# Kernel tuning notes

Measured on AMD Instinct MI355X. Metric: run time of the kernel, lower is better.

## Reference

```python
import jax, jax.numpy as jnp
import numpy as np
import math

H = 2048          # hidden_size
NH = 16           # num_attn_heads
HD = H // NH      # attn head dim = 128
NFW = 4           # num_lact_heads
FD = H // NFW     # fw head dim = 512
DH = FD           # inter_multi = 1.0
CHUNK = 512       # lact_chunk_size
WINDOW = 2048     # window_size
ROPE_BASE = 500000.0
BASE_LR_INV = math.log(math.expm1(0.001))  # inv_softplus(1e-3)


def rmsnorm(x, w, eps=1e-6):
    return x * jax.lax.rsqrt(jnp.mean(x * x, axis=-1, keepdims=True) + eps) * w


def l2norm(x, eps=1e-12):
    return x * jax.lax.rsqrt(jnp.sum(x * x, axis=-1, keepdims=True) + eps)


def rope(x):  # x: [b, h, s, d], half-split convention
    d = x.shape[-1]
    s = x.shape[2]
    inv = 1.0 / (ROPE_BASE ** (jnp.arange(d // 2, dtype=jnp.float32) / (d // 2)))
    f = jnp.arange(s, dtype=jnp.float32)[:, None] * inv[None, :]  # [s, d/2]
    cos, sin = jnp.cos(f), jnp.sin(f)
    x1, x2 = x[..., : d // 2], x[..., d // 2:]
    return jnp.concatenate([x1 * cos - x2 * sin, x2 * cos + x1 * sin], axis=-1)


def setup_inputs() -> dict:
    key = jax.random.key(0)
    ks = jax.random.split(key, 8)
    b, s = 2, 2048
    return {
        "hidden_states": jax.random.normal(ks[0], (b, s, H), jnp.float32),
        "qkv_w": jax.random.normal(ks[1], (3 * H, H), jnp.float32) / math.sqrt(H),
        "q_norm_w": jnp.ones((H,), jnp.float32),
        "k_norm_w": jnp.ones((H,), jnp.float32),
        "qk_scale": jnp.ones((H, 2), jnp.float32),
        "qk_offset": jnp.zeros((H, 2), jnp.float32),
        "lr_w": jax.random.normal(ks[2], (3 * NFW, H), jnp.float32) / math.sqrt(H),
        "lr_b": jnp.zeros((3 * NFW,), jnp.float32),
        "w0": jax.random.normal(ks[3], (NFW, DH, FD), jnp.float32) / math.sqrt(FD),
        "w1": jax.random.normal(ks[4], (NFW, FD, DH), jnp.float32) / math.sqrt(DH),
        "w2": jax.random.normal(ks[5], (NFW, DH, FD), jnp.float32) / math.sqrt(FD),
        "ttt_norm_w": jnp.ones((FD,), jnp.float32),
        "o_proj_w": jax.random.normal(ks[6], (H, H), jnp.float32) / math.sqrt(H),
    }


def reference(hidden_states, qkv_w, q_norm_w, k_norm_w, qk_scale, qk_offset,
              lr_w, lr_b, w0, w1, w2, ttt_norm_w, o_proj_w):
    x = hidden_states
    b, s, _ = x.shape
    nc = s // CHUNK

    qkv = x @ qkv_w.T
    q, k, v = jnp.split(qkv, 3, axis=-1)
    q = rmsnorm(q, q_norm_w)
    k = rmsnorm(k, k_norm_w)

    # ---- TTT (fast-weight SwiGLU) branch ----
    fq = jax.nn.silu(q * qk_scale[:, 0] + qk_offset[:, 0])
    fk = jax.nn.silu(k * qk_scale[:, 1] + qk_offset[:, 1])
    fv = jax.nn.silu(v)
    tohead = lambda t: t.reshape(b, s, NFW, FD).transpose(0, 2, 1, 3)  # [b,h,s,d]
    fq, fk, fv = l2norm(tohead(fq)), l2norm(tohead(fk)), tohead(fv)

    lr = jax.nn.softplus(x @ lr_w.T + lr_b + BASE_LR_INV)          # [b,s,3*NFW]
    lr = lr.reshape(b, s, 3, NFW).transpose(2, 0, 3, 1)[..., None]  # [3,b,h,s,1]
    lr0, lr1, lr2 = lr[0], lr[1], lr[2]

    chunkify = lambda t: t.reshape(b, NFW, nc, CHUNK, -1).transpose(2, 0, 1, 3, 4)
    qs, ks_, vs = chunkify(fq), chunkify(fk), chunkify(fv)
    l0s, l1s, l2s = chunkify(lr0), chunkify(lr1), chunkify(lr2)

    w0b = jnp.broadcast_to(w0, (b,) + w0.shape)
    w1b = jnp.broadcast_to(w1, (b,) + w1.shape)
    w2b = jnp.broadcast_to(w2, (b,) + w2.shape)

    def step(carry, xs):
        w0c, w1c, w2c = carry
        qc, kc, vc, l0, l1, l2 = xs
        # apply current fast weights to queries (strictly causal across chunks)
        hq = jax.nn.silu(jnp.einsum('bhcd,bhed->bhce', qc, w0c)) * \
             jnp.einsum('bhcd,bhed->bhce', qc, w2c)
        oc = jnp.einsum('bhce,bhde->bhcd', hq, w1c)
        # gradient-descent update on dot-product loss -sum(v * f(k))
        g1 = jnp.einsum('bhcd,bhed->bhce', kc, w0c)
        g2 = jnp.einsum('bhcd,bhed->bhce', kc, w2c)
        gate = jax.nn.silu(g1)
        hidden = gate * g2
        dhidden = jnp.einsum('bhcd,bhde->bhce', vc, w1c)  # w1^T v
        dh2 = dhidden * gate
        sig = jax.nn.sigmoid(g1)
        dh1 = dhidden * g2 * (sig * (1.0 + g1 * (1.0 - sig)))  # silu'(g1)
        w1n = w1c + jnp.einsum('bhcd,bhce->bhde', l1 * vc, hidden)
        w0n = w0c + jnp.einsum('bhce,bhcd->bhed', l0 * dh1, kc)
        w2n = w2c + jnp.einsum('bhce,bhcd->bhed', l2 * dh2, kc)
        return (w0n, w1n, w2n), oc

    _, o_chunks = jax.lax.scan(step, (w0b, w1b, w2b), (qs, ks_, vs, l0s, l1s, l2s))
    o_ttt = o_chunks.transpose(1, 2, 0, 3, 4).reshape(b, NFW, s, FD)
    o_ttt = rmsnorm(o_ttt, ttt_norm_w)
    o_ttt = o_ttt.transpose(0, 2, 1, 3).reshape(b, s, H)

    # ---- sliding-window attention branch ----
    qa = rope(q.reshape(b, s, NH, HD).transpose(0, 2, 1, 3))
    ka = rope(k.reshape(b, s, NH, HD).transpose(0, 2, 1, 3))
    va = v.reshape(b, s, NH, HD).transpose(0, 2, 1, 3)
    scores = jnp.einsum('bhqd,bhkd->bhqk', qa, ka) / math.sqrt(HD)
    i = jnp.arange(s)
    mask = (i[:, None] >= i[None, :]) & (i[:, None] - i[None, :] < WINDOW)
    scores = jnp.where(mask, scores, jnp.float32(-1e9))
    p = jax.nn.softmax(scores, axis=-1)
    attn = jnp.einsum('bhqk,bhkd->bhqd', p, va).transpose(0, 2, 1, 3).reshape(b, s, H)

    return (attn + o_ttt) @ o_proj_w.T
```

## Files before the change

### kernel.cpp

```cpp
#include <hip/hip_runtime.h>
#include <hip/hip_bf16.h>
#include <math.h>

using bf16 = __hip_bfloat16;

namespace {

constexpr int cH = 2048;
constexpr int cNH = 16;
constexpr int cHD = 128;
constexpr int cNFW = 4;
constexpr int cFD = 512;
constexpr int cS = 2048;
constexpr float cRSQRT_HD = 0.08838834764831845f;
constexpr long ZL_ = 262144;
constexpr long ZG_ = 1048576;

typedef __attribute__((ext_vector_type(8))) short short8;
typedef __attribute__((ext_vector_type(4))) float f32x4;

__device__ __forceinline__ float sigmoidf_(float x) { return 1.0f / (1.0f + __expf(-x)); }
__device__ __forceinline__ float b2f(bf16 v) { return __bfloat162float(v); }
__device__ __forceinline__ bf16 f2b(float v) { return __float2bfloat16(v); }
__device__ __forceinline__ unsigned short f2bu(float f) {
  return __builtin_bit_cast(unsigned short, __float2bfloat16(f));
}
__device__ __forceinline__ float bu2f(unsigned u) { return __uint_as_float(u << 16); }

#if defined(__has_builtin)
#if __has_builtin(__builtin_amdgcn_global_load_lds)
#define HAVE_GLOAD 1
#endif
#endif

__device__ __forceinline__ void gload16(const bf16* g, short* ldsbase) {
#ifdef HAVE_GLOAD
  __builtin_amdgcn_global_load_lds((const __attribute__((address_space(1))) void*)g,
                                   (__attribute__((address_space(3))) void*)ldsbase, 16, 0, 0);
#else
  const int l = threadIdx.x & 63;
  *(uint4*)(ldsbase + l * 8) = *(const uint4*)g;
#endif
}

__device__ __forceinline__ void stage16(const bf16* src, short* dst) {
  *(uint4*)dst = *(const uint4*)src;
  *(uint4*)(dst + 8) = *(const uint4*)(src + 8);
}

__device__ __forceinline__ void store1(float* p, float v) { *p = v; }
__device__ __forceinline__ void store1(bf16* p, float v) { *p = f2b(v); }

__device__ __forceinline__ void mm_core32(const bf16* __restrict__ Ab, int lda,
                                          const bf16* __restrict__ Bb, int ldb, int K,
                                          short* As, short* Bs, f32x4 acc[4][4]) {
  const int t = threadIdx.x, lane = t & 63, g = lane >> 4, c16 = lane & 15;
  const int wv = t >> 6, wm = (wv >> 1) * 64, wn = (wv & 1) * 64;
  for (int k0 = 0; k0 < K; k0 += 32) {
    __syncthreads();
    {
      const int ch = wv * 2;
      const bf16* ga = Ab + (size_t)(ch * 16 + (lane >> 2)) * lda + k0 + (lane & 3) * 8;
      gload16(ga, &As[ch * 512]);
      gload16(ga + (size_t)16 * lda, &As[ch * 512 + 512]);
      const bf16* gb = Bb + (size_t)(ch * 16 + (lane >> 2)) * ldb + k0 + (lane & 3) * 8;
      gload16(gb, &Bs[ch * 512]);
      gload16(gb + (size_t)16 * ldb, &Bs[ch * 512 + 512]);
    }
    __syncthreads();
    short8 af[4], bfr[4];
#pragma unroll
    for (int mi = 0; mi < 4; ++mi) af[mi] = *(const short8*)&As[(wm + mi * 16 + c16) * 32 + g * 8];
#pragma unroll
    for (int ni = 0; ni < 4; ++ni) bfr[ni] = *(const short8*)&Bs[(wn + ni * 16 + c16) * 32 + g * 8];
#pragma unroll
    for (int mi = 0; mi < 4; ++mi)
#pragma unroll
      for (int ni = 0; ni < 4; ++ni)
        acc[mi][ni] = __builtin_amdgcn_mfma_f32_16x16x32_bf16(af[mi], bfr[ni], acc[mi][ni], 0, 0, 0);
  }
}

template <bool ACC, bool MIR, typename TC>
__device__ __forceinline__ void mm_store(TC* Cb, bf16* Mb, int ldc, int rb, int cb, f32x4 acc[4][4]) {
  const int t = threadIdx.x, lane = t & 63, g = lane >> 4, c16 = lane & 15;
  const int wv = t >> 6, wm = (wv >> 1) * 64, wn = (wv & 1) * 64;
  const int rbase = rb + wm, cbase = cb + wn;
#pragma unroll
  for (int mi = 0; mi < 4; ++mi)
#pragma unroll
    for (int ni = 0; ni < 4; ++ni) {
      const int col = cbase + ni * 16 + c16;
#pragma unroll
      for (int r = 0; r < 4; ++r) {
        const int row = rbase + mi * 16 + g * 4 + r;
        TC* cp = Cb + (size_t)row * ldc + col;
        if constexpr (ACC) {
          float nv = *cp + acc[mi][ni][r];
          *cp = nv;
          if constexpr (MIR) Mb[(size_t)row * ldc + col] = f2b(nv);
        } else {
          store1(cp, acc[mi][ni][r]);
        }
      }
    }
}

template <typename TC>
__global__ __launch_bounds__(512, 1) void k_mm8(const bf16* __restrict__ A, int lda,
                                                const bf16* __restrict__ B, int ldb,
                                                TC* __restrict__ C, int ldc, int K) {
  __shared__ short LA[2][256 * 64];
  __shared__ short LB[2][128 * 64];
  const int t = threadIdx.x, lane = t & 63, wv = t >> 6;
  const int g = lane >> 4, c16 = lane & 15;
  const int wm = (wv >> 1) * 64, wn = (wv & 1) * 64;
  const bf16* Ab = A + (size_t)blockIdx.y * 256 * lda;
  const bf16* Bb = B + (size_t)blockIdx.x * 128 * ldb;
  const int NKT = K >> 6;
  const int srow = wv * 16 + (lane >> 3);
  const int scol = ((lane & 7) ^ ((lane >> 3) & 7)) * 8;

  auto stA = [&](int buf, int half, int kt) {
    const int ktc = (kt < NKT) ? kt : 0;
    const bf16* src = Ab + (size_t)(half * 128 + srow) * lda + ktc * 64 + scol;
    short* dst = &LA[buf][(half * 128 + wv * 16) * 64];
    gload16(src, dst);
    gload16(src + (size_t)8 * lda, dst + 512);
  };
  auto stB = [&](int buf, int kt) {
    const int ktc = (kt < NKT) ? kt : 0;
    const bf16* src = Bb + (size_t)srow * ldb + ktc * 64 + scol;
    short* dst = &LB[buf][(wv * 16) * 64];
    gload16(src, dst);
    gload16(src + (size_t)8 * ldb, dst + 512);
  };

  f32x4 acc[4][4];
  const f32x4 zero4 = {0.f, 0.f, 0.f, 0.f};
#pragma unroll
  for (int i = 0; i < 4; ++i)
#pragma unroll
    for (int j = 0; j < 4; ++j) acc[i][j] = zero4;

  stB(0, 0);
  stA(0, 0, 0);
  stA(0, 1, 0);
  stB(1, 1);
  asm volatile("s_waitcnt vmcnt(0)" ::: "memory");
  __syncthreads();

  const int NITER = NKT >> 1;
  for (int it = 0; it < NITER; ++it) {
    const int T = 2 * it;
#pragma unroll
    for (int hf = 0; hf < 2; ++hf) {
      short8 bfr[4][2];
#pragma unroll
      for (int p = 0; p < 2; ++p) {
        if (p == 0) {
#pragma unroll
          for (int ni = 0; ni < 4; ++ni)
#pragma unroll
            for (int kk = 0; kk < 2; ++kk) {
              const int rb_ = wn + ni * 16 + c16;
              bfr[ni][kk] = *(const short8*)&LB[hf][rb_ * 64 + ((kk * 4 + g) ^ (rb_ & 7)) * 8];
            }
        }
        short8 af[2][2];
#pragma unroll
        for (int j = 0; j < 2; ++j)
#pragma unroll
          for (int kk = 0; kk < 2; ++kk) {
            const int ra_ = wm + (p * 2 + j) * 16 + c16;
            af[j][kk] = *(const short8*)&LA[hf][ra_ * 64 + ((kk * 4 + g) ^ (ra_ & 7)) * 8];
          }
        if (p == 0) {
          stA(hf ^ 1, 0, T + 1 + hf);
        } else {
          stA(hf ^ 1, 1, T + 1 + hf);
          stB(hf, T + 2 + hf);
        }
        asm volatile("" ::: "memory");
        __builtin_amdgcn_s_barrier();
        __builtin_amdgcn_s_setprio(1);
#pragma unroll
        for (int j = 0; j < 2; ++j)
#pragma unroll
          for (int ni = 0; ni < 4; ++ni)
#pragma unroll
            for (int kk = 0; kk < 2; ++kk)
              acc[p * 2 + j][ni] = __builtin_amdgcn_mfma_f32_16x16x32_bf16(
                  af[j][kk], bfr[ni][kk], acc[p * 2 + j][ni], 0, 0, 0);
        __builtin_amdgcn_s_setprio(0);
        if (p == 1) asm volatile("s_waitcnt vmcnt(2)" ::: "memory");
        asm volatile("" ::: "memory");
        __builtin_amdgcn_s_barrier();
      }
    }
  }

  const int rbase = blockIdx.y * 256 + wm, cbase = blockIdx.x * 128 + wn;
#pragma unroll
  for (int fr = 0; fr < 4; ++fr)
#pragma unroll
    for (int ni = 0; ni < 4; ++ni) {
      const int col = cbase + ni * 16 + c16;
#pragma unroll
      for (int r = 0; r < 4; ++r)
        store1(C + (size_t)(rbase + fr * 16 + g * 4 + r) * ldc + col, acc[fr][ni][r]);
    }
}

__global__ __launch_bounds__(256) void k_fuse1(const bf16* __restrict__ fq, const bf16* __restrict__ fk,
                                               const bf16* __restrict__ fv,
                                               const bf16* __restrict__ w0b, const bf16* __restrict__ w1t,
                                               const bf16* __restrict__ w2b,
                                               bf16* __restrict__ hq, bf16* __restrict__ trH,
                                               bf16* __restrict__ trD1, bf16* __restrict__ trD2,
                                               bf16* __restrict__ trK, bf16* __restrict__ trV,
                                               const float* __restrict__ lr0, const float* __restrict__ lr1,
                                               const float* __restrict__ lr2,
                                               const bf16* __restrict__ occ,
                                               const float* __restrict__ tw, bf16* __restrict__ y,
                                               int chunk) {
  __shared__ short S[12288];
  __shared__ float red[4];
  const int id = blockIdx.x, t = threadIdx.x;
  const size_t choff = (size_t)chunk * 262144;

  if (id < 512) {
    const int bh = id >> 6, tile = id & 63, by = tile >> 3, bx = tile & 7;
    const int lane = t & 63, g = lane >> 4, c16 = lane & 15, wv = t >> 6;
    const int wm = (wv >> 1) * 32, wn = (wv & 1) * 32;
    const bf16* Aq = fq + (size_t)bh * ZG_ + choff + (size_t)(by * 64) * cFD;
    const bf16* Ak = fk + (size_t)bh * ZG_ + choff + (size_t)(by * 64) * cFD;
    const bf16* Av = fv + (size_t)bh * ZG_ + choff + (size_t)(by * 64) * cFD;
    const bf16* B0 = w0b + (size_t)bh * ZL_ + (size_t)(bx * 64) * cFD;
    const bf16* B2 = w2b + (size_t)bh * ZL_ + (size_t)(bx * 64) * cFD;
    const bf16* B1 = w1t + (size_t)bh * ZL_ + (size_t)(bx * 64) * cFD;

    f32x4 acc[5][2][2];
    const f32x4 zero4 = {0.f, 0.f, 0.f, 0.f};
#pragma unroll
    for (int v = 0; v < 5; ++v)
#pragma unroll
      for (int i = 0; i < 2; ++i)
#pragma unroll
        for (int j = 0; j < 2; ++j) acc[v][i][j] = zero4;

    const int srow = wv * 16 + (lane >> 2), scol = (lane & 3) * 8;
    for (int k0 = 0; k0 < 512; k0 += 32) {
      __syncthreads();
      gload16(Aq + (size_t)srow * cFD + k0 + scol, &S[0 + wv * 512]);
      gload16(Ak + (size_t)srow * cFD + k0 + scol, &S[2048 + wv * 512]);
      gload16(Av + (size_t)srow * cFD + k0 + scol, &S[4096 + wv * 512]);
      gload16(B0 + (size_t)srow * cFD + k0 + scol, &S[6144 + wv * 512]);
      gload16(B2 + (size_t)srow * cFD + k0 + scol, &S[8192 + wv * 512]);
      gload16(B1 + (size_t)srow * cFD + k0 + scol, &S[10240 + wv * 512]);
      __syncthreads();
      short8 aq[2], ak[2], av[2], b0[2], b2[2], b1[2];
#pragma unroll
      for (int mi = 0; mi < 2; ++mi) {
        const int ro = (wm + mi * 16 + c16) * 32 + g * 8;
        aq[mi] = *(const short8*)&S[0 + ro];
        ak[mi] = *(const short8*)&S[2048 + ro];
        av[mi] = *(const short8*)&S[4096 + ro];
      }
#pragma unroll
      for (int ni = 0; ni < 2; ++ni) {
        const int ro = (wn + ni * 16 + c16) * 32 + g * 8;
        b0[ni] = *(const short8*)&S[6144 + ro];
        b2[ni] = *(const short8*)&S[8192 + ro];
        b1[ni] = *(const short8*)&S[10240 + ro];
      }
#pragma unroll
      for (int mi = 0; mi < 2; ++mi)
#pragma unroll
        for (int ni = 0; ni < 2; ++ni) {
          acc[0][mi][ni] = __builtin_amdgcn_mfma_f32_16x16x32_bf16(aq[mi], b0[ni], acc[0][mi][ni], 0, 0, 0);
          acc[1][mi][ni] = __builtin_amdgcn_mfma_f32_16x16x32_bf16(aq[mi], b2[ni], acc[1][mi][ni], 0, 0, 0);
          acc[2][mi][ni] = __builtin_amdgcn_mfma_f32_16x16x32_bf16(ak[mi], b0[ni], acc[2][mi][ni], 0, 0, 0);
          acc[3][mi][ni] = __builtin_amdgcn_mfma_f32_16x16x32_bf16(ak[mi], b2[ni], acc[3][mi][ni], 0, 0, 0);
          acc[4][mi][ni] = __builtin_amdgcn_mfma_f32_16x16x32_bf16(av[mi], b1[ni], acc[4][mi][ni], 0, 0, 0);
        }
    }

    float l0v[2][4], l2v[2][4];
#pragma unroll
    for (int mi = 0; mi < 2; ++mi)
#pragma unroll
      for (int r = 0; r < 4; ++r) {
        const int row = by * 64 + wm + mi * 16 + g * 4 + r;
        l0v[mi][r] = lr0[bh * 2048 + chunk * 512 + row];
        l2v[mi][r] = lr2[bh * 2048 + chunk * 512 + row];
      }
#pragma unroll
    for (int mi = 0; mi < 2; ++mi)
#pragma unroll
      for (int ni = 0; ni < 2; ++ni)
#pragma unroll
        for (int r = 0; r < 4; ++r) {
          float hq1 = acc[0][mi][ni][r], hq2 = acc[1][mi][ni][r];
          float g1 = acc[2][mi][ni][r], g2 = acc[3][mi][ni][r], dh = acc[4][mi][ni][r];
          acc[0][mi][ni][r] = hq1 * sigmoidf_(hq1) * hq2;
          float sg = sigmoidf_(g1);
          float gate = g1 * sg;
          acc[1][mi][ni][r] = gate * g2;
          acc[2][mi][ni][r] = l0v[mi][r] * dh * g2 * (sg * (1.0f + g1 * (1.0f - sg)));
          acc[3][mi][ni][r] = l2v[mi][r] * dh * gate;
        }

    short* Ts = S;
    bf16* dst0 = hq + (size_t)bh * ZL_;
    bf16* dstT[3] = {trH + (size_t)bh * ZL_, trD1 + (size_t)bh * ZL_, trD2 + (size_t)bh * ZL_};
#pragma unroll
    for (int rd = 0; rd < 4; ++rd) {
      __syncthreads();
#pragma unroll
      for (int mi = 0; mi < 2; ++mi)
#pragma unroll
        for (int ni = 0; ni < 2; ++ni)
#pragma unroll
          for (int r = 0; r < 4; ++r) {
            const int row = wm + mi * 16 + g * 4 + r, col = wn + ni * 16 + c16;
            if (rd == 0) Ts[row * 66 + col] = (short)f2bu(acc[0][mi][ni][r]);
            else Ts[col * 66 + row] = (short)f2bu(acc[rd][mi][ni][r]);
          }
      __syncthreads();
      const int rr = t >> 2, cs = (t & 3) * 16;
      unsigned short u[16] __attribute__((aligned(16)));
#pragma unroll
      for (int i = 0; i < 16; ++i) u[i] = (unsigned short)Ts[rr * 66 + cs + i];
      bf16* dp = (rd == 0) ? (dst0 + (size_t)(by * 64 + rr) * cFD + bx * 64 + cs)
                           : (dstT[rd - 1] + (size_t)(bx * 64 + rr) * cFD + by * 64 + cs);
      *(uint4*)dp = *(uint4*)u;
      *(uint4*)(dp + 8) = *(uint4*)(u + 8);
    }
  } else if (id < 1536) {
    short* Ts = S;
    const int id2 = id - 512;
    const int var = id2 >> 9, bh = (id2 >> 6) & 7, by = (id2 >> 3) & 7, bx = id2 & 7;
    const bf16* src = ((var == 0) ? fk : fv) + choff + (size_t)bh * ZG_;
    bf16* dst = ((var == 0) ? trK : trV) + (size_t)bh * ZL_;
    {
      const int rr = t >> 2, cseg = (t & 3) * 16;
      if (var == 0) {
        stage16(src + (size_t)(by * 64 + rr) * cFD + bx * 64 + cseg, &Ts[rr * 72 + cseg]);
      } else {
        const float s = lr1[bh * 2048 + chunk * 512 + by * 64 + rr];
        const bf16* p = src + (size_t)(by * 64 + rr) * cFD + bx * 64 + cseg;
        unsigned short u[16] __attribute__((aligned(16)));
#pragma unroll
        for (int i = 0; i < 16; ++i) u[i] = f2bu(b2f(p[i]) * s);
        *(uint4*)&Ts[rr * 72 + cseg] = *(uint4*)u;
        *(uint4*)&Ts[rr * 72 + cseg + 8] = *(uint4*)(u + 8);
      }
    }
    __syncthreads();
    {
      const int oc_ = t >> 2, rseg = (t & 3) * 16;
      unsigned short u[16] __attribute__((aligned(16)));
#pragma unroll
      for (int i = 0; i < 16; ++i) u[i] = (unsigned short)Ts[(rseg + i) * 72 + oc_];
      bf16* dp = dst + (size_t)(bx * 64 + oc_) * cFD + by * 64 + rseg;
      *(uint4*)dp = *(uint4*)u;
      *(uint4*)(dp + 8) = *(uint4*)(u + 8);
    }
  } else {
    const int rrow = id - 1536;
    const int bh = rrow >> 9, rr = rrow & 511;
    const bf16* src = occ + ((size_t)bh * 512 + rr) * 512;
    float v0 = b2f(src[t]), v1 = b2f(src[t + 256]);
    float ss = v0 * v0 + v1 * v1;
    for (int d = 32; d; d >>= 1) ss += __shfl_down(ss, d);
    if ((t & 63) == 0) red[t >> 6] = ss;
    __syncthreads();
    const float rstd = rsqrtf((red[0] + red[1] + red[2] + red[3]) / cFD + 1e-6f);
    const int si = (chunk - 1) * 512 + rr;
    bf16* dst = y + ((size_t)((bh >> 2) * cS) + si) * cH + (bh & 3) * cFD;
    dst[t] = f2b(b2f(dst[t]) + v0 * rstd * tw[t]);
    dst[t + 256] = f2b(b2f(dst[t + 256]) + v1 * rstd * tw[t + 256]);
  }
}

__global__ __launch_bounds__(256) void k_updna(const bf16* __restrict__ trV, const bf16* __restrict__ trH,
                                               const bf16* __restrict__ trD1, const bf16* __restrict__ trD2,
                                               const bf16* __restrict__ trK,
                                               const bf16* __restrict__ hq, const bf16* __restrict__ w1bc,
                                               float* w0s, float* w1s, float* w2s,
                                               bf16* w0b, bf16* w1bn, bf16* w2b, bf16* w1t,
                                               bf16* __restrict__ occ) {
  __shared__ short Sh[8704];
  const int id = blockIdx.x, t = threadIdx.x;
  const int lane = t & 63, g = lane >> 4, c16 = lane & 15, wv = t >> 6;
  if (id < 384) {
    short* As = Sh;
    short* Bs = Sh + 4096;
    const int z = id >> 4, tile = id & 15, by = tile >> 2, bx = tile & 3;
    const int var = z >> 3, bh = z & 7;
    const bf16 *Aa, *Bb;
    if (var == 0) {
      Aa = trV + (size_t)bh * ZL_ + (size_t)by * 128 * cFD;
      Bb = trH + (size_t)bh * ZL_ + (size_t)bx * 128 * cFD;
    } else if (var == 1) {
      Aa = trD1 + (size_t)bh * ZL_ + (size_t)by * 128 * cFD;
      Bb = trK + (size_t)bh * ZL_ + (size_t)bx * 128 * cFD;
    } else {
      Aa = trD2 + (size_t)bh * ZL_ + (size_t)by * 128 * cFD;
      Bb = trK + (size_t)bh * ZL_ + (size_t)bx * 128 * cFD;
    }
    f32x4 acc[4][4];
    const f32x4 zero4 = {0.f, 0.f, 0.f, 0.f};
#pragma unroll
    for (int i = 0; i < 4; ++i)
#pragma unroll
      for (int j = 0; j < 4; ++j) acc[i][j] = zero4;
    mm_core32(Aa, cFD, Bb, cFD, cFD, As, Bs, acc);
    if (var == 1) {
      mm_store<true, true>(w0s + (size_t)bh * ZL_, w0b + (size_t)bh * ZL_, cFD, by * 128, bx * 128, acc);
    } else if (var == 2) {
      mm_store<true, true>(w2s + (size_t)bh * ZL_, w2b + (size_t)bh * ZL_, cFD, by * 128, bx * 128, acc);
    } else {
      float* W = w1s + (size_t)bh * ZL_;
      bf16* M = w1bn + (size_t)bh * ZL_;
      const int wm = (wv >> 1) * 64, wn = (wv & 1) * 64;
#pragma unroll
      for (int mi = 0; mi < 4; ++mi)
#pragma unroll
        for (int ni = 0; ni < 4; ++ni) {
          const int col = bx * 128 + wn + ni * 16 + c16;
#pragma unroll
          for (int r = 0; r < 4; ++r) {
            const int row = by * 128 + wm + mi * 16 + g * 4 + r;
            float nv = W[(size_t)row * cFD + col] + acc[mi][ni][r];
            W[(size_t)row * cFD + col] = nv;
            M[(size_t)row * cFD + col] = f2b(nv);
            acc[mi][ni][r] = nv;
          }
        }
      bf16* T = w1t + (size_t)bh * ZL_;
      short* Ts = Sh;
#pragma unroll
      for (int rd = 0; rd < 2; ++rd) {
        __syncthreads();
        if (wn == rd * 64) {
#pragma unroll
          for (int mi = 0; mi < 4; ++mi)
#pragma unroll
            for (int ni = 0; ni < 4; ++ni) {
              const int cc = ni * 16 + c16;
              unsigned short u[4] __attribute__((aligned(8)));
#pragma unroll
              for (int r = 0; r < 4; ++r) u[r] = f2bu(acc[mi][ni][r]);
              *(uint2*)&Ts[cc * 136 + wm + mi * 16 + g * 4] = *(uint2*)u;
            }
        }
        __syncthreads();
        const int cc = t >> 2, seg = (t & 3) * 32;
        unsigned short u[32] __attribute__((aligned(16)));
#pragma unroll
        for (int i = 0; i < 32; ++i) u[i] = (unsigned short)Ts[cc * 136 + seg + i];
        bf16* dp = T + (size_t)(bx * 128 + rd * 64 + cc) * cFD + by * 128 + seg;
        *(uint4*)dp = *(uint4*)u;
        *(uint4*)(dp + 8) = *(uint4*)(u + 8);
        *(uint4*)(dp + 16) = *(uint4*)(u + 16);
        *(uint4*)(dp + 24) = *(uint4*)(u + 24);
      }
    }
  } else {
    short* As = Sh;
    short* Bs = Sh + 4096;
    const int id2 = id - 384;
    const int bh = id2 >> 4, tile = id2 & 15, by = tile >> 2, bx = tile & 3;
    const bf16* Aa = hq + (size_t)bh * ZL_ + (size_t)by * 128 * cFD;
    const bf16* Bb = w1bc + (size_t)bh * ZL_ + (size_t)bx * 128 * cFD;
    f32x4 acc[4][4];
    const f32x4 zero4 = {0.f, 0.f, 0.f, 0.f};
#pragma unroll
    for (int i = 0; i < 4; ++i)
#pragma unroll
      for (int j = 0; j < 4; ++j) acc[i][j] = zero4;
    mm_core32(Aa, cFD, Bb, cFD, cFD, As, Bs, acc);
    mm_store<false, false>(occ + (size_t)bh * ZL_, (bf16*)nullptr, cFD, by * 128, bx * 128, acc);
  }
}

__global__ __launch_bounds__(256) void k_normcvt(const bf16* __restrict__ occ,
                                                 const float* __restrict__ tw, bf16* __restrict__ y,
                                                 const float* __restrict__ opw, bf16* __restrict__ opwb,
                                                 int chunk) {
  __shared__ float red[4];
  const int id = blockIdx.x, t = threadIdx.x;
  if (id < 4096) {
    const int bh = id >> 9, rr = id & 511;
    const bf16* src = occ + ((size_t)bh * 512 + rr) * 512;
    float v0 = b2f(src[t]), v1 = b2f(src[t + 256]);
    float ss = v0 * v0 + v1 * v1;
    for (int d = 32; d; d >>= 1) ss += __shfl_down(ss, d);
    if ((t & 63) == 0) red[t >> 6] = ss;
    __syncthreads();
    const float rstd = rsqrtf((red[0] + red[1] + red[2] + red[3]) / cFD + 1e-6f);
    const int si = chunk * 512 + rr;
    bf16* dst = y + ((size_t)((bh >> 2) * cS) + si) * cH + (bh & 3) * cFD;
    dst[t] = f2b(b2f(dst[t]) + v0 * rstd * tw[t]);
    dst[t + 256] = f2b(b2f(dst[t + 256]) + v1 * rstd * tw[t + 256]);
  } else {
    const size_t i = ((size_t)(id - 4096) * 256 + t) * 8;
    float4 a = *(const float4*)(opw + i), b = *(const float4*)(opw + i + 4);
    unsigned short u[8] __attribute__((aligned(16)));
    u[0] = f2bu(a.x); u[1] = f2bu(a.y); u[2] = f2bu(a.z); u[3] = f2bu(a.w);
    u[4] = f2bu(b.x); u[5] = f2bu(b.y); u[6] = f2bu(b.z); u[7] = f2bu(b.w);
    *(uint4*)(opwb + i) = *(uint4*)u;
  }
}

__global__ __launch_bounds__(256) void k_prep(const float* __restrict__ x, const float* __restrict__ qkv_w,
                                              const float* __restrict__ w0, const float* __restrict__ w1,
                                              const float* __restrict__ w2,
                                              const float* __restrict__ lr_w, const float* __restrict__ lr_b,
                                              bf16* __restrict__ xb, bf16* __restrict__ qkvwb,
                                              float* __restrict__ w0s, float* __restrict__ w1s,
                                              float* __restrict__ w2s,
                                              float* __restrict__ ct, float* __restrict__ stb,
                                              float* lr0, float* lr1, float* lr2, float base) {
  __shared__ float xbuf[cH];
  const int id = blockIdx.x, t = threadIdx.x;
  if (id < 4096) {
    const size_t i = ((size_t)id * 256 + t) * 8;
    float4 a = *(const float4*)(x + i), b = *(const float4*)(x + i + 4);
    unsigned short u[8] __attribute__((aligned(16)));
    u[0] = f2bu(a.x); u[1] = f2bu(a.y); u[2] = f2bu(a.z); u[3] = f2bu(a.w);
    u[4] = f2bu(b.x); u[5] = f2bu(b.y); u[6] = f2bu(b.z); u[7] = f2bu(b.w);
    *(uint4*)(xb + i) = *(uint4*)u;
  } else if (id < 10240) {
    const size_t i = ((size_t)(id - 4096) * 256 + t) * 8;
    float4 a = *(const float4*)(qkv_w + i), b = *(const float4*)(qkv_w + i + 4);
    unsigned short u[8] __attribute__((aligned(16)));
    u[0] = f2bu(a.x); u[1] = f2bu(a.y); u[2] = f2bu(a.z); u[3] = f2bu(a.w);
    u[4] = f2bu(b.x); u[5] = f2bu(b.y); u[6] = f2bu(b.z); u[7] = f2bu(b.w);
    *(uint4*)(qkvwb + i) = *(uint4*)u;
  } else if (id < 16384) {
    const int sub = id - 10240;
    const int w = sub >> 11, blk = sub & 2047;
    const size_t i = ((size_t)blk * 256 + t) * 4;
    const int f = (int)((i >> 18) & 3);
    const size_t off = i & 262143;
    const float* src = (w == 0) ? w0 : (w == 1) ? w1 : w2;
    float* dst = (w == 0) ? w0s : (w == 1) ? w1s : w2s;
    *(float4*)(dst + i) = *(const float4*)(src + (size_t)f * 262144 + off);
  } else if (id < 16896) {
    const int gid = (id - 16384) * 256 + t;
    const int si = gid >> 6, jj = gid & 63;
    float inv = powf(500000.0f, -(float)jj / 64.0f);
    float ang = (float)si * inv;
    ct[(size_t)si * 64 + jj] = cosf(ang);
    stb[(size_t)si * 64 + jj] = sinf(ang);
  } else {
    const int token = id - 16896, b_ = token >> 11, si = token & 2047;
    const int wv = t >> 6, lane = t & 63;
    const float* xr = x + (size_t)token * cH;
    for (int i = t; i < cH; i += 256) xbuf[i] = xr[i];
    __syncthreads();
#pragma unroll
    for (int jj = 0; jj < 3; ++jj) {
      const int j = wv * 3 + jj;
      const float* wr = lr_w + (size_t)j * cH;
      float s = 0.f;
      for (int k = lane; k < cH; k += 64) s += xbuf[k] * wr[k];
      for (int d = 32; d; d >>= 1) s += __shfl_down(s, d);
      if (lane == 0) {
        float v = s + lr_b[j] + base;
        float sp = (v > 15.f) ? v : log1pf(expf(v));
        const int tt = j >> 2, f = j & 3;
        float* dst = (tt == 0 ? lr0 : tt == 1 ? lr1 : lr2);
        dst[(size_t)(b_ * cNFW + f) * cS + si] = sp;
      }
    }
  }
}

__global__ __launch_bounds__(256) void k_post2(bf16* __restrict__ qkvh,
                                               const float* __restrict__ qnw, const float* __restrict__ knw,
                                               const float* __restrict__ ct, const float* __restrict__ stb,
                                               bf16* __restrict__ qa, bf16* __restrict__ ka,
                                               bf16* __restrict__ vt) {
  __shared__ short smem[8704];
  __shared__ float red[4];
  const int id = blockIdx.x, t = threadIdx.x;
  if (id < 4096) {
    float* buf = (float*)smem;
    const int token = id, b_ = token >> 11, si = token & 2047;
    bf16* base = qkvh + (size_t)token * 3 * cH;
    for (int pass = 0; pass < 2; ++pass) {
      __syncthreads();
      bf16* src = base + pass * cH;
      const float* nw = pass ? knw : qnw;
      float ss = 0.f;
      for (int i = t; i < cH; i += 256) {
        float v = b2f(src[i]);
        buf[i] = v;
        ss += v * v;
      }
      for (int d = 32; d; d >>= 1) ss += __shfl_down(ss, d);
      if ((t & 63) == 0) red[t >> 6] = ss;
      __syncthreads();
      const float rstd = rsqrtf((red[0] + red[1] + red[2] + red[3]) / cH + 1e-6f);
      for (int i = t; i < cH; i += 256) {
        float v = buf[i] * rstd * nw[i];
        buf[i] = v;
        src[i] = f2b(v);
      }
      __syncthreads();
      bf16* dst = pass ? ka : qa;
      const float scale = pass ? 1.f : cRSQRT_HD;
      const int hh = t >> 4, j0 = (t & 15) * 4;
      const float* cr = ct + (size_t)si * 64 + j0;
      const float* sr = stb + (size_t)si * 64 + j0;
      bf16* drow = dst + ((size_t)(b_ * cNH + hh) * cS + si) * cHD;
      unsigned short u1[4] __attribute__((aligned(8))), u2[4] __attribute__((aligned(8)));
#pragma unroll
      for (int i = 0; i < 4; ++i) {
        float x1 = buf[hh * cHD + j0 + i], x2 = buf[hh * cHD + 64 + j0 + i];
        u1[i] = f2bu((x1 * cr[i] - x2 * sr[i]) * scale);
        u2[i] = f2bu((x2 * cr[i] + x1 * sr[i]) * scale);
      }
      *(uint2*)(drow + j0) = *(uint2*)u1;
      *(uint2*)(drow + 64 + j0) = *(uint2*)u2;
    }
  } else {
    short* Ts = smem;
    const int id2 = id - 4096;
    const int tile = id2 & 31, h = (id2 >> 5) & 15, b_ = id2 >> 9;
    {
      const int r = t >> 2, seg = (t & 3) * 32;
      const bf16* src = qkvh + ((size_t)(b_ * cS) + tile * 64 + r) * 3 * cH + 2 * cH + h * cHD + seg;
      stage16(src, &Ts[r * 136 + seg]);
      stage16(src + 16, &Ts[r * 136 + seg + 16]);
    }
    __syncthreads();
    {
      const int d = t >> 1, seg2 = (t & 1) * 32;
      unsigned short u[32] __attribute__((aligned(16)));
#pragma unroll
      for (int i = 0; i < 32; ++i) u[i] = (unsigned short)Ts[(seg2 + i) * 136 + d];
      bf16* dp = vt + ((size_t)(b_ * cNH + h) * cHD + d) * cS + tile * 64 + seg2;
      *(uint4*)dp = *(uint4*)u;
      *(uint4*)(dp + 8) = *(uint4*)(u + 8);
      *(uint4*)(dp + 16) = *(uint4*)(u + 16);
      *(uint4*)(dp + 24) = *(uint4*)(u + 24);
    }
  }
}

__global__ __launch_bounds__(256) void k_mid(const bf16* __restrict__ qkvh,
                                             const float* __restrict__ qk_scale,
                                             const float* __restrict__ qk_offset,
                                             bf16* fq, bf16* fk, bf16* fv,
                                             const float* __restrict__ w0s_, bf16* __restrict__ w0b_,
                                             const float* __restrict__ w1s_, bf16* __restrict__ w1t_) {
  __shared__ short Ts[64 * 72];
  const int id = blockIdx.x, t = threadIdx.x;
  if (id < 4096) {
    const int token = id, b_ = token >> 11, si = token & 2047;
    const bf16* base = qkvh + (size_t)token * 3 * cH;
#pragma unroll
    for (int pass = 0; pass < 2; ++pass) {
      const bf16* src = base + pass * cH;
      bf16* fdst = pass ? fk : fq;
      const int head = t >> 6, lane = t & 63;
      float f[8];
      float ss2 = 0.f;
#pragma unroll
      for (int k = 0; k < 8; ++k) {
        const int idx = head * cFD + lane + k * 64;
        float v = b2f(src[idx]);
        float u = v * qk_scale[idx * 2 + pass] + qk_offset[idx * 2 + pass];
        float fv_ = u * sigmoidf_(u);
        f[k] = fv_;
        ss2 += fv_ * fv_;
      }
      for (int d = 1; d < 64; d <<= 1) ss2 += __shfl_xor(ss2, d);
      const float sc2 = rsqrtf(ss2 + 1e-12f);
      bf16* dst = fdst + ((size_t)(b_ * cNFW + head) * cS + si) * cFD;
#pragma unroll
      for (int k = 0; k < 8; ++k) dst[lane + k * 64] = f2b(f[k] * sc2);
    }
    const bf16* vr = base + 2 * cH;
    for (int i = t; i < cH; i += 256) {
      float v = b2f(vr[i]);
      fv[((size_t)(b_ * cNFW + (i >> 9)) * cS + si) * cFD + (i & 511)] = f2b(v * sigmoidf_(v));
    }
  } else if (id < 7168) {
    const size_t i = ((size_t)(id - 4096) * 256 + t) * 8;
    float4 a = *(const float4*)(w0s_ + i), b = *(const float4*)(w0s_ + i + 4);
    unsigned short u[8] __attribute__((aligned(16)));
    u[0] = f2bu(a.x); u[1] = f2bu(a.y); u[2] = f2bu(a.z); u[3] = f2bu(a.w);
    u[4] = f2bu(b.x); u[5] = f2bu(b.y); u[6] = f2bu(b.z); u[7] = f2bu(b.w);
    *(uint4*)(w0b_ + i) = *(uint4*)u;
  } else {
    const int id3 = id - 7168;
    const int bh = id3 >> 6, tile = id3 & 63, by = tile >> 3, bx = tile & 7;
    {
      const int rr = t >> 2, cseg = (t & 3) * 16;
      const float* p = w1s_ + (size_t)bh * ZL_ + (size_t)(by * 64 + rr) * cFD + bx * 64 + cseg;
      unsigned short u[16] __attribute__((aligned(16)));
#pragma unroll
      for (int i = 0; i < 16; ++i) u[i] = f2bu(p[i]);
      *(uint4*)&Ts[rr * 72 + cseg] = *(uint4*)u;
      *(uint4*)&Ts[rr * 72 + cseg + 8] = *(uint4*)(u + 8);
    }
    __syncthreads();
    {
      const int oc_ = t >> 2, rseg = (t & 3) * 16;
      unsigned short u[16] __attribute__((aligned(16)));
#pragma unroll
      for (int i = 0; i < 16; ++i) u[i] = (unsigned short)Ts[(rseg + i) * 72 + oc_];
      bf16* dp = w1t_ + (size_t)bh * ZL_ + (size_t)(bx * 64 + oc_) * cFD + by * 64 + rseg;
      *(uint4*)dp = *(uint4*)u;
      *(uint4*)(dp + 8) = *(uint4*)(u + 8);
    }
  }
}

__global__ __launch_bounds__(512) void k_attn6(const bf16* __restrict__ qa, const bf16* __restrict__ ka,
                                               const bf16* __restrict__ vt, bf16* __restrict__ y) {
  const int id = blockIdx.x;
  const int xcd = id & 7;
  const int j = id >> 3;
  const int p = j & 7;
  const int hb = (j >> 3) * 8 + xcd;
  const int h = hb & 15, b_ = hb >> 4;
  __shared__ short KsP[9216];
  __shared__ short Vts[128 * 72];
  const int t = threadIdx.x, lane = t & 63, g = lane >> 4, c16 = lane & 15, wv = t >> 6;
  const size_t hbq = (size_t)(b_ * cNH + h) * cS;
  const bf16* vb = vt + (size_t)(b_ * cNH + h) * (size_t)(cHD * cS);
  const int r = t >> 3, seg = (t & 7) * 16;
  const int dv = t >> 2, seg2 = (t & 3) * 16;
  const f32x4 zero4 = {0.f, 0.f, 0.f, 0.f};

  for (int half = 0; half < 2; ++half) {
    const int qt = half ? p : 15 - p;
    const int q0 = qt * 128;
    const int nkt = 2 * qt + 2;
    short8 qf[4];
    {
      const bf16* qsrc = qa + (hbq + q0 + wv * 16 + c16) * cHD;
#pragma unroll
      for (int ks = 0; ks < 4; ++ks) qf[ks] = *(const short8*)(qsrc + ks * 32 + g * 8);
    }
    f32x4 o[8];
#pragma unroll
    for (int i = 0; i < 8; ++i) o[i] = zero4;
    float m[4], l[4];
#pragma unroll
    for (int rr = 0; rr < 4; ++rr) { m[rr] = -1e30f; l[rr] = 0.f; }

    uint4 kp0, kp1, vp0, vp1;
    {
      const bf16* ksrc = ka + (hbq + r) * cHD + seg;
      kp0 = *(const uint4*)ksrc; kp1 = *(const uint4*)(ksrc + 8);
      const bf16* vsrc = vb + (size_t)dv * cS + seg2;
      vp0 = *(const uint4*)vsrc; vp1 = *(const uint4*)(vsrc + 8);
    }

    for (int kt = 0; kt < nkt; ++kt) {
      __syncthreads();
      {
        short* kd = &KsP[r * 136 + seg];
        *(uint4*)kd = kp0; *(uint4*)(kd + 8) = kp1;
        short* vd = &Vts[dv * 72 + seg2];
        *(uint4*)vd = vp0; *(uint4*)(vd + 8) = vp1;
      }
      __syncthreads();
      if (kt + 1 < nkt) {
        const bf16* ksrc = ka + (hbq + (kt + 1) * 64 + r) * cHD + seg;
        kp0 = *(const uint4*)ksrc; kp1 = *(const uint4*)(ksrc + 8);
        const bf16* vsrc = vb + (size_t)dv * cS + (kt + 1) * 64 + seg2;
        vp0 = *(const uint4*)vsrc; vp1 = *(const uint4*)(vsrc + 8);
      } else if (half == 0) {
        const bf16* ksrc = ka + (hbq + r) * cHD + seg;
        kp0 = *(const uint4*)ksrc; kp1 = *(const uint4*)(ksrc + 8);
        const bf16* vsrc = vb + (size_t)dv * cS + seg2;
        vp0 = *(const uint4*)vsrc; vp1 = *(const uint4*)(vsrc + 8);
      }

      f32x4 s4[4];
#pragma unroll
      for (int ni = 0; ni < 4; ++ni) s4[ni] = zero4;
      __builtin_amdgcn_s_setprio(1);
#pragma unroll
      for (int ks = 0; ks < 4; ++ks) {
#pragma unroll
        for (int ni = 0; ni < 4; ++ni) {
          short8 bb = *(const short8*)&KsP[(ni * 16 + c16) * 136 + ks * 32 + g * 8];
          s4[ni] = __builtin_amdgcn_mfma_f32_16x16x32_bf16(qf[ks], bb, s4[ni], 0, 0, 0);
        }
      }
      __builtin_amdgcn_s_setprio(0);
      __syncthreads();
      if (kt * 64 + 64 > q0) {
#pragma unroll
        for (int ni = 0; ni < 4; ++ni) {
          const int kv = kt * 64 + ni * 16 + c16;
#pragma unroll
          for (int rr = 0; rr < 4; ++rr) {
            const int qr = q0 + wv * 16 + g * 4 + rr;
            if (kv > qr) s4[ni][rr] = -1e9f;
          }
        }
      }
      float mx[4];
#pragma unroll
      for (int rr = 0; rr < 4; ++rr)
        mx[rr] = fmaxf(fmaxf(s4[0][rr], s4[1][rr]), fmaxf(s4[2][rr], s4[3][rr]));
#pragma unroll
      for (int d = 1; d < 16; d <<= 1)
#pragma unroll
        for (int rr = 0; rr < 4; ++rr) mx[rr] = fmaxf(mx[rr], __shfl_xor(mx[rr], d));
      bool need = false;
#pragma unroll
      for (int rr = 0; rr < 4; ++rr) need |= (mx[rr] > m[rr] + 8.f);
      if (__any(need)) {
        float corr[4];
#pragma unroll
        for (int rr = 0; rr < 4; ++rr) {
          float mn = fmaxf(m[rr], mx[rr]);
          corr[rr] = __expf(m[rr] - mn);
          m[rr] = mn;
        }
#pragma unroll
        for (int rr = 0; rr < 4; ++rr) l[rr] *= corr[rr];
#pragma unroll
        for (int nf = 0; nf < 8; ++nf)
#pragma unroll
          for (int rr = 0; rr < 4; ++rr) o[nf][rr] *= corr[rr];
      }
      float psum[4] = {0.f, 0.f, 0.f, 0.f};
#pragma unroll
      for (int ni = 0; ni < 4; ++ni)
#pragma unroll
        for (int rr = 0; rr < 4; ++rr) {
          float pp = __expf(s4[ni][rr] - m[rr]);
          s4[ni][rr] = pp;
          psum[rr] += pp;
        }
#pragma unroll
      for (int d = 1; d < 16; d <<= 1)
#pragma unroll
        for (int rr = 0; rr < 4; ++rr) psum[rr] += __shfl_xor(psum[rr], d);
#pragma unroll
      for (int rr = 0; rr < 4; ++rr) l[rr] += psum[rr];
      short* pw = &KsP[wv * 1152];
#pragma unroll
      for (int ni = 0; ni < 4; ++ni)
#pragma unroll
        for (int rr = 0; rr < 4; ++rr)
          pw[(g * 4 + rr) * 72 + ni * 16 + c16] = (short)f2bu(s4[ni][rr]);
      __builtin_amdgcn_s_setprio(1);
#pragma unroll
      for (int ks2 = 0; ks2 < 2; ++ks2) {
        short8 a = *(const short8*)&pw[c16 * 72 + ks2 * 32 + g * 8];
#pragma unroll
        for (int nf = 0; nf < 8; ++nf) {
          short8 bb = *(const short8*)&Vts[(nf * 16 + c16) * 72 + ks2 * 32 + g * 8];
          o[nf] = __builtin_amdgcn_mfma_f32_16x16x32_bf16(a, bb, o[nf], 0, 0, 0);
        }
      }
      __builtin_amdgcn_s_setprio(0);
    }
    float inv[4];
#pragma unroll
    for (int rr = 0; rr < 4; ++rr) inv[rr] = 1.f / l[rr];
#pragma unroll
    for (int nf = 0; nf < 8; ++nf)
#pragma unroll
      for (int rr = 0; rr < 4; ++rr) {
        const size_t row = (size_t)(b_ * cS) + q0 + wv * 16 + g * 4 + rr;
        y[row * cH + h * cHD + nf * 16 + c16] = f2b(o[nf][rr] * inv[rr]);
      }
  }
}

}

extern "C" void kernel_launch(void* const* d_in, const int* in_sizes, int n_in,
                              void* d_out, int out_size, void* d_ws, size_t ws_size,
                              hipStream_t stream) {
  (void)in_sizes; (void)n_in; (void)out_size; (void)ws_size;
  const float* x         = (const float*)d_in[0];
  const float* qkv_w     = (const float*)d_in[1];
  const float* q_norm_w  = (const float*)d_in[2];
  const float* k_norm_w  = (const float*)d_in[3];
  const float* qk_scale  = (const float*)d_in[4];
  const float* qk_offset = (const float*)d_in[5];
  const float* lr_w      = (const float*)d_in[6];
  const float* lr_b      = (const float*)d_in[7];
  const float* w0        = (const float*)d_in[8];
  const float* w1        = (const float*)d_in[9];
  const float* w2        = (const float*)d_in[10];
  const float* ttt_nw    = (const float*)d_in[11];
  const float* o_proj_w  = (const float*)d_in[12];
  float* out = (float*)d_out;

  char* Wb = (char*)d_ws;
  bf16* qkvh = (bf16*)Wb;
  bf16* hq   = (bf16*)(Wb + 0UL);
  bf16* trH  = (bf16*)(Wb + 4194304UL);
  bf16* trD1 = (bf16*)(Wb + 8388608UL);
  bf16* trD2 = (bf16*)(Wb + 12582912UL);
  bf16* trK  = (bf16*)(Wb + 16777216UL);
  bf16* trV  = (bf16*)(Wb + 20971520UL);
  bf16* occ  = (bf16*)(Wb + 25165824UL);
  bf16* w1t  = (bf16*)(Wb + 29360128UL);
  bf16* w0b  = (bf16*)(Wb + 33554432UL);
  bf16* w1b0 = (bf16*)(Wb + 37748736UL);
  bf16* w2b  = (bf16*)(Wb + 41943040UL);
  bf16* w1b1 = (bf16*)(Wb + 46137344UL);
  bf16* opwb = (bf16*)(Wb + 0UL);
  size_t off = 50331648UL;
  bf16* fqb = (bf16*)(Wb + off); off += 16777216UL;
  bf16* fkb = (bf16*)(Wb + off); off += 16777216UL;
  bf16* fvb = (bf16*)(Wb + off); off += 16777216UL;
  float* w0s = (float*)(Wb + off); off += 8388608UL;
  float* w1s = (float*)(Wb + off); off += 8388608UL;
  float* w2s = (float*)(Wb + off); off += 8388608UL;
  float* lr0 = (float*)(Wb + off); off += 65536UL;
  float* lr1 = (float*)(Wb + off); off += 65536UL;
  float* lr2 = (float*)(Wb + off); off += 65536UL;
  bf16* y = (bf16*)(Wb + off); off += 16777216UL;
  float* ct  = (float*)(Wb + off); off += 524288UL;
  float* stb = (float*)(Wb + off); off += 524288UL;
  bf16* xb = fqb;
  bf16* qkvwb = fkb;
  bf16* qa = fqb;
  bf16* ka = fkb;
  bf16* vt = fvb;
  bf16* w1m[2] = {w1b0, w1b1};

  const float base_lr_inv = logf(expm1f(0.001f));
  dim3 blk(256);

  k_prep<<<dim3(20992), blk, 0, stream>>>(x, qkv_w, w0, w1, w2, lr_w, lr_b,
                                          xb, qkvwb, w0s, w1s, w2s, ct, stb,
                                          lr0, lr1, lr2, base_lr_inv);
  k_mm8<bf16><<<dim3(48, 16), dim3(512), 0, stream>>>(xb, 2048, qkvwb, 2048, qkvh, 6144, 2048);
  k_post2<<<dim3(5120), blk, 0, stream>>>(qkvh, q_norm_w, k_norm_w, ct, stb, qa, ka, vt);
  k_attn6<<<dim3(256), dim3(512), 0, stream>>>(qa, ka, vt, y);
  k_mid<<<dim3(7680), blk, 0, stream>>>(qkvh, qk_scale, qk_offset, fqb, fkb, fvb,
                                        w0s, w0b, w1s, w1t);

  for (int c = 0; c < 4; ++c) {
    const int g1 = (c == 0) ? 1536 : 5632;
    k_fuse1<<<dim3(g1), blk, 0, stream>>>(fqb, fkb, fvb, w0b, w1t, w2b,
                                          hq, trH, trD1, trD2, trK, trV,
                                          lr0, lr1, lr2, occ, ttt_nw, y, c);
    k_updna<<<dim3(512), blk, 0, stream>>>(trV, trH, trD1, trD2, trK, hq, w1m[c & 1],
                                           w0s, w1s, w2s, w0b, w1m[(c + 1) & 1], w2b, w1t,
                                           occ);
  }
  k_normcvt<<<dim3(6144), blk, 0, stream>>>(occ, ttt_nw, y, o_proj_w, opwb, 3);
  k_mm8<float><<<dim3(16, 16), dim3(512), 0, stream>>>(y, 2048, opwb, 2048, out, 2048, 2048);
}
```

Baseline: 682.6 us.

## Triple-buffer LDS in k_mm8 GEMM with one barrier per k-tile

Replaces the double-buffered, half-step ping-pong pipeline in the bf16 MFMA GEMM with a three-stage LDS ring buffer. Each k-tile loads all A and B fragments, issues global-to-LDS loads two tiles ahead, runs the MFMAs, then waits with vmcnt(6) and a single barrier. This removes the extra barriers and the split A-half scheduling, and gives loads a longer prefetch distance to hide memory latency. In exchange, LDS use grows by half to about 147KB per block, and more fragment registers are live at once.

```diff
diff --git a/kernel.cpp b/kernel.cpp
--- a/kernel.cpp
+++ b/kernel.cpp
@@ -110,8 +110,8 @@
 __global__ __launch_bounds__(512, 1) void k_mm8(const bf16* __restrict__ A, int lda,
                                                 const bf16* __restrict__ B, int ldb,
                                                 TC* __restrict__ C, int ldc, int K) {
-  __shared__ short LA[2][256 * 64];
-  __shared__ short LB[2][128 * 64];
+  __shared__ short LA[3][256 * 64];
+  __shared__ short LB[3][128 * 64];
   const int t = threadIdx.x, lane = t & 63, wv = t >> 6;
   const int g = lane >> 4, c16 = lane & 15;
   const int wm = (wv >> 1) * 64, wn = (wv & 1) * 64;
@@ -143,61 +143,36 @@
 #pragma unroll
     for (int j = 0; j < 4; ++j) acc[i][j] = zero4;
 
-  stB(0, 0);
-  stA(0, 0, 0);
-  stA(0, 1, 0);
-  stB(1, 1);
-  asm volatile("s_waitcnt vmcnt(0)" ::: "memory");
-  __syncthreads();
-
-  const int NITER = NKT >> 1;
-  for (int it = 0; it < NITER; ++it) {
-    const int T = 2 * it;
-#pragma unroll
-    for (int hf = 0; hf < 2; ++hf) {
-      short8 bfr[4][2];
-#pragma unroll
-      for (int p = 0; p < 2; ++p) {
-        if (p == 0) {
-#pragma unroll
-          for (int ni = 0; ni < 4; ++ni)
-#pragma unroll
-            for (int kk = 0; kk < 2; ++kk) {
-              const int rb_ = wn + ni * 16 + c16;
-              bfr[ni][kk] = *(const short8*)&LB[hf][rb_ * 64 + ((kk * 4 + g) ^ (rb_ & 7)) * 8];
-            }
-        }
-        short8 af[2][2];
-#pragma unroll
-        for (int j = 0; j < 2; ++j)
-#pragma unroll
-          for (int kk = 0; kk < 2; ++kk) {
-            const int ra_ = wm + (p * 2 + j) * 16 + c16;
-            af[j][kk] = *(const short8*)&LA[hf][ra_ * 64 + ((kk * 4 + g) ^ (ra_ & 7)) * 8];
-          }
-        if (p == 0) {
-          stA(hf ^ 1, 0, T + 1 + hf);
-        } else {
-          stA(hf ^ 1, 1, T + 1 + hf);
-          stB(hf, T + 2 + hf);
-        }
-        asm volatile("" ::: "memory");
-        __builtin_amdgcn_s_barrier();
-        __builtin_amdgcn_s_setprio(1);
-#pragma unroll
-        for (int j = 0; j < 2; ++j)
-#pragma unroll
-          for (int ni = 0; ni < 4; ++ni)
-#pragma unroll
-            for (int kk = 0; kk < 2; ++kk)
-              acc[p * 2 + j][ni] = __builtin_amdgcn_mfma_f32_16x16x32_bf16(
-                  af[j][kk], bfr[ni][kk], acc[p * 2 + j][ni], 0, 0, 0);
-        __builtin_amdgcn_s_setprio(0);
-        if (p == 1) asm volatile("s_waitcnt vmcnt(2)" ::: "memory");
-        asm volatile("" ::: "memory");
-        __builtin_amdgcn_s_barrier();
-      }
-    }
+  stA(0, 0, 0); stA(0, 1, 0); stB(0, 0);
+  stA(1, 0, 1); stA(1, 1, 1); stB(1, 1);
+  asm volatile("s_waitcnt vmcnt(6)" ::: "memory");
+  __builtin_amdgcn_s_barrier();
+
+  for (int kt = 0; kt < NKT; ++kt) {
+    const int cb = kt % 3, nb = (kt + 2) % 3;
+    short8 af[4][2], bfr[4][2];
+#pragma unroll
+    for (int f = 0; f < 4; ++f)
+#pragma unroll
+      for (int kk = 0; kk < 2; ++kk) {
+        const int ra = wm + f * 16 + c16;
+        af[f][kk] = *(const short8*)&LA[cb][ra * 64 + ((kk * 4 + g) ^ (ra & 7)) * 8];
+        const int rb_ = wn + f * 16 + c16;
+        bfr[f][kk] = *(const short8*)&LB[cb][rb_ * 64 + ((kk * 4 + g) ^ (rb_ & 7)) * 8];
+      }
+    stA(nb, 0, kt + 2); stA(nb, 1, kt + 2); stB(nb, kt + 2);
+    __builtin_amdgcn_s_setprio(1);
+#pragma unroll
+    for (int f = 0; f < 4; ++f)
+#pragma unroll
+      for (int ni = 0; ni < 4; ++ni)
+#pragma unroll
+        for (int kk = 0; kk < 2; ++kk)
+          acc[f][ni] = __builtin_amdgcn_mfma_f32_16x16x32_bf16(
+              af[f][kk], bfr[ni][kk], acc[f][ni], 0, 0, 0);
+    __builtin_amdgcn_s_setprio(0);
+    asm volatile("s_waitcnt vmcnt(6)" ::: "memory");
+    __builtin_amdgcn_s_barrier();
   }
 
   const int rbase = blockIdx.y * 256 + wm, cbase = blockIdx.x * 128 + wn;
```

Measured after the change: 660.8 us, median of 2. -3.2%, faster.
